# Performance work log

Hardware: AMD Instinct MI355X
Metric: run time of the kernel (lower is better)

Reference implementation:

```python
import math
import jax, jax.numpy as jnp
import numpy as np

B, N = 8, 2048
IN_DIM = COND_DIM = ATTN_DIM = OUT_DIM = 128
NUM_HEADS = 4
DH = ATTN_DIM // NUM_HEADS  # 32


def setup_inputs() -> dict:
    key = jax.random.key(0)
    ks = jax.random.split(key, 10)
    s_in = 1.0 / math.sqrt(IN_DIM)
    s_cd = 1.0 / math.sqrt(COND_DIM)
    return {
        "x": jax.random.normal(ks[0], (B, N, IN_DIM), jnp.float32),
        "cond": jax.random.normal(ks[1], (B, N, COND_DIM), jnp.float32),
        "flags": jnp.ones((B, N, 1), jnp.float32),
        "attention_mask": jax.random.normal(ks[2], (B, N, N), jnp.float32),
        # Linear params (stored [in, out]; torch Linear is x @ W.T + b)
        "Wq": jax.random.uniform(ks[3], (IN_DIM, ATTN_DIM), jnp.float32, -s_in, s_in),
        "bq": jax.random.uniform(ks[4], (ATTN_DIM,), jnp.float32, -s_in, s_in),
        "Wk": jax.random.uniform(ks[5], (COND_DIM, ATTN_DIM), jnp.float32, -s_cd, s_cd),
        "bk": jax.random.uniform(ks[6], (ATTN_DIM,), jnp.float32, -s_cd, s_cd),
        "Wv": jax.random.uniform(ks[7], (COND_DIM, OUT_DIM), jnp.float32, -s_cd, s_cd),
        "bv": jax.random.uniform(ks[8], (OUT_DIM,), jnp.float32, -s_cd, s_cd),
    }


def reference(x, cond, flags, attention_mask, Wq, bq, Wk, bk, Wv, bv):
    # flags is accepted but unused, matching the original forward.
    b, n, _ = x.shape
    Q = (x @ Wq + bq).reshape(b, n, NUM_HEADS, DH)     # channel-split heads
    K = (cond @ Wk + bk).reshape(b, n, NUM_HEADS, DH)
    V = cond @ Wv + bv                                 # [B, N, OUT_DIM]
    # per-head scores, scaled by sqrt(out_dim) as in the original
    S = jnp.einsum("bnhd,bmhd->hbnm", Q, K) / math.sqrt(OUT_DIM)
    A = jnp.tanh(attention_mask[None] + S)             # tanh activation, not softmax
    A = A.mean(axis=0)                                 # head-mean -> [B, N, N]
    return jnp.einsum("bnm,bmd->bnd", A, V)
```

## Files before the change

### kernel.cpp

```cpp
#include <hip/hip_runtime.h>
#include <hip/hip_bf16.h>

typedef __attribute__((ext_vector_type(4))) float f32x4;
typedef __attribute__((ext_vector_type(8))) short bf16x8;

#define MFMA16(A, B, C) __builtin_amdgcn_mfma_f32_16x16x32_bf16(A, B, C, 0, 0, 0)

#define C2 2.8853900817779268f
#define QS (2.8853900817779268f / 11.313708498984761f)

__device__ __forceinline__ unsigned cvtpk_bf16(float lo, float hi) {
    unsigned r;
    asm("v_cvt_pk_bf16_f32 %0, %1, %2" : "=v"(r) : "v"(lo), "v"(hi));
    return r;
}

__device__ __forceinline__ bf16x8 pack8(float4 a, float4 b) {
    union { unsigned u[4]; bf16x8 v; } u;
    u.u[0] = cvtpk_bf16(a.x, a.y);
    u.u[1] = cvtpk_bf16(a.z, a.w);
    u.u[2] = cvtpk_bf16(b.x, b.y);
    u.u[3] = cvtpk_bf16(b.z, b.w);
    return u.v;
}

__device__ __forceinline__ void gload_lds16(const void* g, void* l) {
    __builtin_amdgcn_global_load_lds(
        (const __attribute__((address_space(1))) unsigned int*)g,
        (__attribute__((address_space(3))) unsigned int*)l, 16, 0, 0);
}

__global__ void prep_weights(const float* __restrict__ Wq, const float* __restrict__ bq,
                             const float* __restrict__ Wk, const float* __restrict__ bk,
                             const float* __restrict__ Wv, const float* __restrict__ bv,
                             __hip_bfloat16* __restrict__ Wqt, __hip_bfloat16* __restrict__ Wkt,
                             __hip_bfloat16* __restrict__ Wvt, float* __restrict__ bias) {
    int i = blockIdx.x * 256 + threadIdx.x;
    int k = i >> 7, o = i & 127;
    Wqt[o * 128 + k] = __float2bfloat16(Wq[i] * QS);
    Wkt[o * 128 + k] = __float2bfloat16(Wk[i]);
    Wvt[o * 128 + k] = __float2bfloat16(Wv[i] * 0.25f);
    if (i < 128) {
        bias[i]       = bq[i] * QS;
        bias[128 + i] = bk[i];
        bias[256 + i] = bv[i] * 0.25f;
    }
}

__global__ __launch_bounds__(256) void proj_qkv(
        const float* __restrict__ x, const float* __restrict__ cond,
        const __hip_bfloat16* __restrict__ Wqt, const __hip_bfloat16* __restrict__ Wkt,
        const __hip_bfloat16* __restrict__ Wvt, const float* __restrict__ bias,
        __hip_bfloat16* __restrict__ Qo, __hip_bfloat16* __restrict__ Ko,
        __hip_bfloat16* __restrict__ Vt) {
    const int lane = threadIdx.x & 63, wv = threadIdx.x >> 6;
    const int l15 = lane & 15, g = lane >> 4;
    const int row0 = blockIdx.x * 64 + wv * 16;

    f32x4 qa[8], ka[8], va[8];
#pragma unroll
    for (int ot = 0; ot < 8; ++ot) {
        float b0 = bias[16 * ot + l15];
        float b1 = bias[128 + 16 * ot + l15];
        float b2 = bias[256 + 16 * ot + l15];
        qa[ot] = (f32x4){b0, b0, b0, b0};
        ka[ot] = (f32x4){b1, b1, b1, b1};
        va[ot] = (f32x4){b2, b2, b2, b2};
    }

    const float* xp = x    + (size_t)(row0 + l15) * 128 + 8 * g;
    const float* cp = cond + (size_t)(row0 + l15) * 128 + 8 * g;
#pragma unroll
    for (int kk = 0; kk < 4; ++kk) {
        float4 x0 = *(const float4*)(xp + 32 * kk);
        float4 x1 = *(const float4*)(xp + 32 * kk + 4);
        float4 c0 = *(const float4*)(cp + 32 * kk);
        float4 c1 = *(const float4*)(cp + 32 * kk + 4);
        bf16x8 xa = pack8(x0, x1);
        bf16x8 ca = pack8(c0, c1);
#pragma unroll
        for (int ot = 0; ot < 8; ++ot) {
            const int wo = (16 * ot + l15) * 128 + 32 * kk + 8 * g;
            qa[ot] = MFMA16(xa, *(const bf16x8*)(Wqt + wo), qa[ot]);
            ka[ot] = MFMA16(ca, *(const bf16x8*)(Wkt + wo), ka[ot]);
            va[ot] = MFMA16(ca, *(const bf16x8*)(Wvt + wo), va[ot]);
        }
    }

#pragma unroll
    for (int ot = 0; ot < 8; ++ot)
#pragma unroll
        for (int r = 0; r < 4; ++r) {
            size_t idx = (size_t)(row0 + 4 * g + r) * 128 + 16 * ot + l15;
            Qo[idx] = __float2bfloat16(qa[ot][r]);
            Ko[idx] = __float2bfloat16(ka[ot][r]);
        }
    const int bb = row0 >> 11, nn = (row0 & 2047) + 4 * g;
#pragma unroll
    for (int ot = 0; ot < 8; ++ot) {
        uint2 pr;
        pr.x = cvtpk_bf16(va[ot][0], va[ot][1]);
        pr.y = cvtpk_bf16(va[ot][2], va[ot][3]);
        *(uint2*)((unsigned short*)Vt + ((size_t)bb * 128 + 16 * ot + l15) * 2048 + nn) = pr;
    }
}

__global__ __launch_bounds__(512) void attn_main(
        const __hip_bfloat16* __restrict__ Q, const __hip_bfloat16* __restrict__ K,
        const __hip_bfloat16* __restrict__ Vt, const float* __restrict__ mask,
        float* __restrict__ out) {
    __shared__ __align__(16) char Kl[2][8192];
    __shared__ __align__(16) char Vl[2][8192];
    __shared__ __align__(16) char Al[64 * 72];

    const int lane = threadIdx.x & 63, w = threadIdx.x >> 6;
    const int l15 = lane & 15, g = lane >> 4;
    const int qw = w & 3, mw = w >> 2, dw = mw;
    const int qt = blockIdx.x & 31;
    const int mh = (blockIdx.x >> 5) & 1;
    const int b  = blockIdx.x >> 6;
    const int n0 = qt * 64;
    const int mh0 = mh * 1024;

    const __hip_bfloat16* Qb = Q + ((size_t)b * 2048 + n0 + qw * 16) * 128;
    const char* Kg = (const char*)(K + (size_t)b * 2048 * 128);
    const char* Vg = (const char*)(Vt + (size_t)b * 128 * 2048);
    const float* mrow = mask + ((size_t)b * 2048 + n0 + qw * 16 + l15) * 2048
                        + mh0 + mw * 16 + 4 * g;

    bf16x8 qf[4];
#pragma unroll
    for (int h = 0; h < 4; ++h)
        qf[h] = *(const bf16x8*)(Qb + l15 * 128 + 32 * h + 8 * g);

    f32x4 oacc[4];
#pragma unroll
    for (int dtl = 0; dtl < 4; ++dtl) oacc[dtl] = (f32x4){0.f, 0.f, 0.f, 0.f};
    const f32x4 zero = (f32x4){0.f, 0.f, 0.f, 0.f};

    auto STAGE = [&](int m0g, int bi) {
        const int o = w * 1024 + lane * 16;
        const int kr = o >> 8, kc = o & 255;
        gload_lds16(Kg + (size_t)(m0g + kr) * 256 + (kc ^ ((kr & 15) << 4)),
                    &Kl[bi][w * 1024]);
        const int vr = o >> 6, vc = o & 63;
        gload_lds16(Vg + (size_t)vr * 4096 + (size_t)m0g * 2 + (vc ^ ((vr & 3) << 4)),
                    &Vl[bi][w * 1024]);
    };

    STAGE(mh0, 0);
    f32x4 mkc = *(const f32x4*)(mrow);
    asm volatile("s_waitcnt vmcnt(0)" ::: "memory");
    __builtin_amdgcn_s_barrier();

#pragma unroll 2
    for (int c = 0; c < 32; ++c) {
        const int bi = c & 1;
        f32x4 mkn;
        if (c < 31) {
            STAGE(mh0 + (c + 1) * 32, bi ^ 1);
            mkn = *(const f32x4*)(mrow + (c + 1) * 32);
        }

        {
            const int mr = mw * 16 + l15;
            const char* kb = &Kl[bi][mr * 256];
            const int sw = l15 << 4;
            f32x4 s0 = MFMA16(*(const bf16x8*)(kb + ((g * 16) ^ sw)),       qf[0], zero);
            f32x4 s1 = MFMA16(*(const bf16x8*)(kb + ((64 + g * 16) ^ sw)),  qf[1], zero);
            f32x4 s2 = MFMA16(*(const bf16x8*)(kb + ((128 + g * 16) ^ sw)), qf[2], zero);
            f32x4 s3 = MFMA16(*(const bf16x8*)(kb + ((192 + g * 16) ^ sw)), qf[3], zero);
            float acd[4];
#pragma unroll
            for (int r = 0; r < 4; ++r) {
                float m2 = mkc[r] * C2;
                float e0 = __builtin_amdgcn_exp2f(m2 + s0[r]);
                float e1 = __builtin_amdgcn_exp2f(m2 + s1[r]);
                float e2 = __builtin_amdgcn_exp2f(m2 + s2[r]);
                float e3 = __builtin_amdgcn_exp2f(m2 + s3[r]);
                float rs = __builtin_amdgcn_rcpf(1.f + e0) + __builtin_amdgcn_rcpf(1.f + e1)
                         + __builtin_amdgcn_rcpf(1.f + e2) + __builtin_amdgcn_rcpf(1.f + e3);
                acd[r] = 4.f - 2.f * rs;
            }
            uint2 pk;
            pk.x = cvtpk_bf16(acd[0], acd[1]);
            pk.y = cvtpk_bf16(acd[2], acd[3]);
            *(uint2*)(Al + (qw * 16 + l15) * 72 + (mw * 16 + 4 * g) * 2) = pk;
        }

        asm volatile("s_waitcnt lgkmcnt(0)" ::: "memory");
        __builtin_amdgcn_s_barrier();

        {
            bf16x8 af = *(const bf16x8*)(Al + (qw * 16 + l15) * 72 + g * 16);
#pragma unroll
            for (int dtl = 0; dtl < 4; ++dtl) {
                const int dr = dw * 64 + dtl * 16 + l15;
                bf16x8 vf = *(const bf16x8*)(
                    &Vl[bi][dr * 64 + ((g * 16) ^ ((dr & 3) << 4))]);
                oacc[dtl] = MFMA16(af, vf, oacc[dtl]);
            }
        }

        asm volatile("s_waitcnt vmcnt(0)" ::: "memory");
        __builtin_amdgcn_s_barrier();
        mkc = mkn;
    }

    float* ob = out + ((size_t)b * 2048 + n0 + qw * 16) * 128 + dw * 64;
#pragma unroll
    for (int dtl = 0; dtl < 4; ++dtl)
#pragma unroll
        for (int r = 0; r < 4; ++r)
            unsafeAtomicAdd(&ob[(size_t)(4 * g + r) * 128 + dtl * 16 + l15], oacc[dtl][r]);
}

extern "C" void kernel_launch(void* const* d_in, const int* in_sizes, int n_in,
                              void* d_out, int out_size, void* d_ws, size_t ws_size,
                              hipStream_t stream) {
    const float* x    = (const float*)d_in[0];
    const float* cond = (const float*)d_in[1];
    const float* mask = (const float*)d_in[3];
    const float* Wq = (const float*)d_in[4];
    const float* bq = (const float*)d_in[5];
    const float* Wk = (const float*)d_in[6];
    const float* bk = (const float*)d_in[7];
    const float* Wv = (const float*)d_in[8];
    const float* bv = (const float*)d_in[9];
    float* out = (float*)d_out;

    char* ws = (char*)d_ws;
    __hip_bfloat16* Qo  = (__hip_bfloat16*)(ws);
    __hip_bfloat16* Ko  = (__hip_bfloat16*)(ws + (4  << 20));
    __hip_bfloat16* Vt  = (__hip_bfloat16*)(ws + (8  << 20));
    __hip_bfloat16* Wqt = (__hip_bfloat16*)(ws + (12 << 20));
    __hip_bfloat16* Wkt = (__hip_bfloat16*)(ws + (12 << 20) + 32768);
    __hip_bfloat16* Wvt = (__hip_bfloat16*)(ws + (12 << 20) + 65536);
    float*          bias = (float*)(ws + (12 << 20) + 98304);

    hipMemsetAsync(d_out, 0, (size_t)out_size * sizeof(float), stream);

    prep_weights<<<64, 256, 0, stream>>>(Wq, bq, Wk, bk, Wv, bv, Wqt, Wkt, Wvt, bias);
    proj_qkv<<<256, 256, 0, stream>>>(x, cond, Wqt, Wkt, Wvt, bias, Qo, Ko, Vt);
    attn_main<<<512, 512, 0, stream>>>(Qo, Ko, Vt, mask, out);
}
```

Baseline: 91.24 us.

## Software-pipeline PV of previous chunk with score computation, triple-buffer V

Reworks the main loop so the A·V MFMA for chunk c-1 runs in the same phase as the score and tanh computation for chunk c. This removes the mid-iteration barrier and lgkmcnt wait, leaving one barrier per chunk. The A tile is now double-buffered and V is triple-buffered, with an epilogue that handles the last chunk. The cost is extra LDS (about 49KB per block), which may limit how many blocks fit per CU.

```diff
diff --git a/kernel.cpp b/kernel.cpp
--- a/kernel.cpp
+++ b/kernel.cpp
@@ -110,8 +110,8 @@
         const __hip_bfloat16* __restrict__ Vt, const float* __restrict__ mask,
         float* __restrict__ out) {
     __shared__ __align__(16) char Kl[2][8192];
-    __shared__ __align__(16) char Vl[2][8192];
-    __shared__ __align__(16) char Al[64 * 72];
+    __shared__ __align__(16) char Vl[3][8192];
+    __shared__ __align__(16) char Al[2][4608];
 
     const int lane = threadIdx.x & 63, w = threadIdx.x >> 6;
     const int l15 = lane & 15, g = lane >> 4;
@@ -138,33 +138,36 @@
     for (int dtl = 0; dtl < 4; ++dtl) oacc[dtl] = (f32x4){0.f, 0.f, 0.f, 0.f};
     const f32x4 zero = (f32x4){0.f, 0.f, 0.f, 0.f};
 
-    auto STAGE = [&](int m0g, int bi) {
+    auto STAGE = [&](int m0g, int kb, int vb) {
         const int o = w * 1024 + lane * 16;
         const int kr = o >> 8, kc = o & 255;
         gload_lds16(Kg + (size_t)(m0g + kr) * 256 + (kc ^ ((kr & 15) << 4)),
-                    &Kl[bi][w * 1024]);
+                    &Kl[kb][w * 1024]);
         const int vr = o >> 6, vc = o & 63;
         gload_lds16(Vg + (size_t)vr * 4096 + (size_t)m0g * 2 + (vc ^ ((vr & 3) << 4)),
-                    &Vl[bi][w * 1024]);
+                    &Vl[vb][w * 1024]);
     };
 
-    STAGE(mh0, 0);
+    STAGE(mh0, 0, 0);
     f32x4 mkc = *(const f32x4*)(mrow);
     asm volatile("s_waitcnt vmcnt(0)" ::: "memory");
     __builtin_amdgcn_s_barrier();
 
+    int vb_st = 1;
+    int vb_pv = 2;
+
 #pragma unroll 2
     for (int c = 0; c < 32; ++c) {
-        const int bi = c & 1;
+        const int abi = c & 1;
         f32x4 mkn;
         if (c < 31) {
-            STAGE(mh0 + (c + 1) * 32, bi ^ 1);
+            STAGE(mh0 + (c + 1) * 32, abi ^ 1, vb_st);
             mkn = *(const f32x4*)(mrow + (c + 1) * 32);
         }
 
         {
             const int mr = mw * 16 + l15;
-            const char* kb = &Kl[bi][mr * 256];
+            const char* kb = &Kl[abi][mr * 256];
             const int sw = l15 << 4;
             f32x4 s0 = MFMA16(*(const bf16x8*)(kb + ((g * 16) ^ sw)),       qf[0], zero);
             f32x4 s1 = MFMA16(*(const bf16x8*)(kb + ((64 + g * 16) ^ sw)),  qf[1], zero);
@@ -185,26 +188,37 @@
             uint2 pk;
             pk.x = cvtpk_bf16(acd[0], acd[1]);
             pk.y = cvtpk_bf16(acd[2], acd[3]);
-            *(uint2*)(Al + (qw * 16 + l15) * 72 + (mw * 16 + 4 * g) * 2) = pk;
-        }
-
-        asm volatile("s_waitcnt lgkmcnt(0)" ::: "memory");
-        __builtin_amdgcn_s_barrier();
-
-        {
-            bf16x8 af = *(const bf16x8*)(Al + (qw * 16 + l15) * 72 + g * 16);
+            *(uint2*)(&Al[abi][(qw * 16 + l15) * 72 + (mw * 16 + 4 * g) * 2]) = pk;
+        }
+
+        if (c > 0) {
+            bf16x8 af = *(const bf16x8*)(&Al[abi ^ 1][(qw * 16 + l15) * 72 + g * 16]);
 #pragma unroll
             for (int dtl = 0; dtl < 4; ++dtl) {
                 const int dr = dw * 64 + dtl * 16 + l15;
                 bf16x8 vf = *(const bf16x8*)(
-                    &Vl[bi][dr * 64 + ((g * 16) ^ ((dr & 3) << 4))]);
+                    &Vl[vb_pv][dr * 64 + ((g * 16) ^ ((dr & 3) << 4))]);
                 oacc[dtl] = MFMA16(af, vf, oacc[dtl]);
             }
         }
 
-        asm volatile("s_waitcnt vmcnt(0)" ::: "memory");
+        asm volatile("s_waitcnt vmcnt(0) lgkmcnt(0)" ::: "memory");
         __builtin_amdgcn_s_barrier();
+
         mkc = mkn;
+        vb_st = (vb_st == 2) ? 0 : vb_st + 1;
+        vb_pv = (vb_pv == 2) ? 0 : vb_pv + 1;
+    }
+
+    {
+        bf16x8 af = *(const bf16x8*)(&Al[1][(qw * 16 + l15) * 72 + g * 16]);
+#pragma unroll
+        for (int dtl = 0; dtl < 4; ++dtl) {
+            const int dr = dw * 64 + dtl * 16 + l15;
+            bf16x8 vf = *(const bf16x8*)(
+                &Vl[vb_pv][dr * 64 + ((g * 16) ^ ((dr & 3) << 4))]);
+            oacc[dtl] = MFMA16(af, vf, oacc[dtl]);
+        }
     }
 
     float* ob = out + ((size_t)b * 2048 + n0 + qw * 16) * 128 + dw * 64;
```

After: 88.87 us. -2.6%, faster.
